# Kernel tuning notes

Measured on AMD Instinct MI355X. Metric: run time of the kernel, lower is better.

Reference implementation:

```python
import jax, jax.numpy as jnp
import numpy as np

B, N, M = 32, 32, 64          # batch, timesteps, local group length (group_token_length+3)
NL, NG = 192, 768             # n_embd_local, n_embd_global
HL, HG = 6, 12                # n_head_local, n_head_global


def setup_inputs() -> dict:
    key = jax.random.key(0)
    ks = jax.random.split(key, 16)
    def w(k, shape, s=0.02):
        return jax.random.normal(k, shape, jnp.float32) * s
    inp = {}
    inp["xl"] = jax.random.normal(ks[0], (B, N, M, NL), jnp.float32)
    inp["xg"] = jax.random.normal(ks[1], (B, 2 * N, NG), jnp.float32)
    i = 2
    for pre, d in (("l", NL), ("g", NG)):
        inp[f"{pre}_ln1_w"] = jnp.ones((d,), jnp.float32)
        inp[f"{pre}_ln1_b"] = jnp.zeros((d,), jnp.float32)
        inp[f"{pre}_ln2_w"] = jnp.ones((d,), jnp.float32)
        inp[f"{pre}_ln2_b"] = jnp.zeros((d,), jnp.float32)
        for nm in ("q", "k", "v", "o"):
            inp[f"{pre}_w{nm}"] = w(ks[i], (d, d)); i += 1
            inp[f"{pre}_b{nm}"] = jnp.zeros((d,), jnp.float32)
        inp[f"{pre}_w1"] = w(ks[i], (d, 4 * d)); i += 1
        inp[f"{pre}_b1"] = jnp.zeros((4 * d,), jnp.float32)
        inp[f"{pre}_w2"] = w(ks[i], (4 * d, d)); i += 1
        inp[f"{pre}_b2"] = jnp.zeros((d,), jnp.float32)
    inp["d_w"] = w(ks[i], (M * NL, NG))
    inp["d_b"] = jnp.zeros((NG,), jnp.float32)
    return inp


def _ln(x, g, b):
    m = x.mean(-1, keepdims=True)
    v = ((x - m) ** 2).mean(-1, keepdims=True)
    return (x - m) / jnp.sqrt(v + 1e-5) * g + b


def _attn(x, wq, bq, wk, bk, wv, bv, wo, bo, nh, allow):
    # x: [B', L, D]; allow: [L, L] bool (True = attend)
    Bx, L, D = x.shape
    hd = D // nh
    q = (x @ wq + bq).reshape(Bx, L, nh, hd)
    k = (x @ wk + bk).reshape(Bx, L, nh, hd)
    v = (x @ wv + bv).reshape(Bx, L, nh, hd)
    s = jnp.einsum('bihd,bjhd->bhij', q, k) / np.float32(np.sqrt(hd))
    s = jnp.where(allow[None, None], s, -jnp.inf)
    p = jax.nn.softmax(s, axis=-1)
    y = jnp.einsum('bhij,bjhd->bihd', p, v).reshape(Bx, L, D)
    return y @ wo + bo


def _tblock(x, p, nh, allow):
    (ln1w, ln1b, ln2w, ln2b, wq, bq, wk, bk, wv, bv, wo, bo, w1, b1, w2, b2) = p
    x = x + _attn(_ln(x, ln1w, ln1b), wq, bq, wk, bk, wv, bv, wo, bo, nh, allow)
    h = _ln(x, ln2w, ln2b)
    return x + (jax.nn.gelu(h @ w1 + b1, approximate=False) @ w2 + b2)


def reference(xl, xg,
              l_ln1_w, l_ln1_b, l_ln2_w, l_ln2_b,
              l_wq, l_bq, l_wk, l_bk, l_wv, l_bv, l_wo, l_bo,
              l_w1, l_b1, l_w2, l_b2,
              g_ln1_w, g_ln1_b, g_ln2_w, g_ln2_b,
              g_wq, g_bq, g_wk, g_bk, g_wv, g_bv, g_wo, g_bo,
              g_w1, g_b1, g_w2, g_b2,
              d_w, d_b):
    Bx, Nx, Mx, nl = xl.shape
    ng = xg.shape[-1]
    lp = (l_ln1_w, l_ln1_b, l_ln2_w, l_ln2_b, l_wq, l_bq, l_wk, l_bk,
          l_wv, l_bv, l_wo, l_bo, l_w1, l_b1, l_w2, l_b2)
    gp = (g_ln1_w, g_ln1_b, g_ln2_w, g_ln2_b, g_wq, g_bq, g_wk, g_bk,
          g_wv, g_bv, g_wo, g_bo, g_w1, g_b1, g_w2, g_b2)

    # local block: causal attention within each group of M tokens
    allow_l = jnp.tril(jnp.ones((Mx, Mx), bool))
    x = _tblock(xl.reshape(Bx * Nx, Mx, nl), lp, HL, allow_l)
    xl_out = x.reshape(Bx, Nx, Mx, nl)

    # summarize each group into one global token, interleave with xg pairs
    zg = (xl_out.reshape(Bx, Nx, Mx * nl) @ d_w + d_b)[:, :, None, :]  # [B,N,1,ng]
    zg = jnp.concatenate([zg, xg.reshape(Bx, Nx, 2, ng)], axis=2)      # [B,N,3,ng]
    zg = zg.reshape(Bx, 3 * Nx, ng)

    # global mask: tril plus within-triplet upper entries; the global block
    # additionally applies its own causal mask, so combined = causal & custom
    L = 3 * Nx
    idx = jnp.arange(L)
    causal = idx[:, None] >= idx[None, :]
    custom = causal | (idx[:, None] // 3 == idx[None, :] // 3)
    allow_g = causal & custom

    zg = _tblock(zg, gp, HG, allow_g)
    xg_out = zg.reshape(Bx, Nx, 3, ng)[:, :, 1:, :].reshape(Bx, 2 * Nx, ng)
    return (xl_out, xg_out)
```

## Files before the change

kernel.cpp:

```cpp
#include <hip/hip_runtime.h>
#include <hip/hip_bf16.h>


typedef unsigned short ushort;
typedef __bf16 bf16x8 __attribute__((ext_vector_type(8)));
typedef float f32x4 __attribute__((ext_vector_type(4)));

__device__ __forceinline__ float us2f(ushort u) {
  union { unsigned i; float f; } w; w.i = ((unsigned)u) << 16; return w.f;
}
__device__ __forceinline__ ushort f2us(float f) {
  __hip_bfloat16 h = __float2bfloat16(f);
  return *reinterpret_cast<ushort*>(&h);
}
__device__ __forceinline__ float gelu_exact(float v) {
  return 0.5f * v * (1.f + erff(v * 0.70710678118654752f));
}
__device__ __forceinline__ void gload16(const ushort* g, ushort* l) {
  __builtin_amdgcn_global_load_lds(
      (const __attribute__((address_space(1))) void*)g,
      (__attribute__((address_space(3))) void*)l, 16, 0, 0);
}

__global__ __launch_bounds__(256)
void transp_kernel(const float* __restrict__ W, ushort* __restrict__ Wt,
                   int K, int N, int dstStride, int rowOff)
{
  __shared__ float t[64][65];
  int n0 = blockIdx.x * 64, k0 = blockIdx.y * 64;
  int c = threadIdx.x & 63, r = threadIdx.x >> 6;
  #pragma unroll
  for (int i = 0; i < 16; ++i) {
    int kr = r + i * 4;
    t[kr][c] = W[(size_t)(k0 + kr) * N + n0 + c];
  }
  __syncthreads();
  #pragma unroll
  for (int i = 0; i < 16; ++i) {
    int nr = r + i * 4;
    Wt[(size_t)(rowOff + n0 + nr) * dstStride + k0 + c] = f2us(t[c][nr]);
  }
}

__global__ __launch_bounds__(256)
void pack3_kernel(float* dst, const float* a, int na, const float* b, int nb,
                  const float* c, int nc)
{
  int i = blockIdx.x * 256 + threadIdx.x;
  if (i >= na + nb + nc) return;
  dst[i] = (i < na) ? a[i] : (i < na + nb ? b[i - na] : c[i - na - nb]);
}

template<int D>
__global__ __launch_bounds__(256)
void ln_kernel(const float* __restrict__ x, const float* __restrict__ g,
               const float* __restrict__ bb, ushort* __restrict__ out, int rows)
{
  int wave = threadIdx.x >> 6, lane = threadIdx.x & 63;
  int row = blockIdx.x * 4 + wave;
  if (row >= rows) return;
  const float* xr = x + (size_t)row * D;
  constexpr int E = D / 64;
  float vals[E];
  float s = 0.f;
  #pragma unroll
  for (int e = 0; e < E; ++e) { vals[e] = xr[e * 64 + lane]; s += vals[e]; }
  #pragma unroll
  for (int off = 32; off >= 1; off >>= 1) s += __shfl_xor(s, off);
  float m = s * (1.f / D);
  float s2 = 0.f;
  #pragma unroll
  for (int e = 0; e < E; ++e) { float d = vals[e] - m; s2 += d * d; }
  #pragma unroll
  for (int off = 32; off >= 1; off >>= 1) s2 += __shfl_xor(s2, off);
  float rstd = rsqrtf(s2 * (1.f / D) + 1e-5f);
  ushort* orow = out + (size_t)row * D;
  #pragma unroll
  for (int e = 0; e < E; ++e) {
    int c = e * 64 + lane;
    orow[c] = f2us((vals[e] - m) * rstd * g[c] + bb[c]);
  }
}

template<int ACT, int RES, int OUTF, int OUTB, int BIAS, int SPLITK>
__global__ __launch_bounds__(256)
void mgemm(const ushort* __restrict__ A, const ushort* __restrict__ Bt,
           const float* __restrict__ bias, const float* __restrict__ resF,
           float* __restrict__ Cf, ushort* __restrict__ Cb,
           int M, int N, int K, int kChunk)
{
  __shared__ __align__(16) ushort Asm[128 * 32];
  __shared__ __align__(16) ushort Bsm[64 * 32];
  const int tid = threadIdx.x;
  const int wave = tid >> 6, lane = tid & 63;
  const int quad = lane >> 4, lm = lane & 15;
  const int rowBase = blockIdx.y * 128, colBase = blockIdx.x * 64;
  const int wrow = (wave & 1) * 64, wcol = (wave >> 1) * 32;
  const int srow = lane >> 2, skcol = (lane & 3) * 8;

  f32x4 acc[4][2] = {};
  const int kbeg = SPLITK ? blockIdx.z * kChunk : 0;
  const int kend = kbeg + (SPLITK ? kChunk : K);

  for (int k0 = kbeg; k0 < kend; k0 += 32) {
    #pragma unroll
    for (int uu = 0; uu < 3; ++uu) {
      int u = wave * 3 + uu;
      if (u < 8) {
        const ushort* gp = A + (size_t)(rowBase + u * 16 + srow) * K + k0 + skcol;
        gload16(gp, &Asm[u * 512]);
      } else {
        int v = u - 8;
        const ushort* gp = Bt + (size_t)(colBase + v * 16 + srow) * K + k0 + skcol;
        gload16(gp, &Bsm[v * 512]);
      }
    }
    __syncthreads();
    bf16x8 af[4], bfr[2];
    #pragma unroll
    for (int r2 = 0; r2 < 4; ++r2)
      af[r2] = *reinterpret_cast<const bf16x8*>(&Asm[(wrow + r2 * 16 + lm) * 32 + quad * 8]);
    #pragma unroll
    for (int c2 = 0; c2 < 2; ++c2)
      bfr[c2] = *reinterpret_cast<const bf16x8*>(&Bsm[(wcol + c2 * 16 + lm) * 32 + quad * 8]);
    #pragma unroll
    for (int r2 = 0; r2 < 4; ++r2)
      #pragma unroll
      for (int c2 = 0; c2 < 2; ++c2)
        acc[r2][c2] = __builtin_amdgcn_mfma_f32_16x16x32_bf16(af[r2], bfr[c2], acc[r2][c2], 0, 0, 0);
    __syncthreads();
  }

  const size_t zoff = SPLITK ? (size_t)blockIdx.z * M * N : 0;
  #pragma unroll
  for (int r2 = 0; r2 < 4; ++r2) {
    #pragma unroll
    for (int c2 = 0; c2 < 2; ++c2) {
      int col = colBase + wcol + c2 * 16 + lm;
      int row0 = rowBase + wrow + r2 * 16 + quad * 4;
      #pragma unroll
      for (int g = 0; g < 4; ++g) {
        float v = acc[r2][c2][g];
        size_t idx = (size_t)(row0 + g) * N + col;
        if (BIAS) v += bias[col];
        if (ACT == 1) v = gelu_exact(v);
        if (RES) v += resF[idx];
        if (OUTF) Cf[zoff + idx] = v;
        if (OUTB) Cb[idx] = f2us(v);
      }
    }
  }
}

__global__ __launch_bounds__(256)
void reduce8_kernel(const float* __restrict__ P, const float* __restrict__ db,
                    float* __restrict__ ZG)
{
  int i = blockIdx.x * 256 + threadIdx.x;
  float s = db[i % 768];
  #pragma unroll
  for (int k = 0; k < 8; ++k) s += P[i + k * 786432];
  ZG[i] = s;
}

template<int L, int HD, int NW>
__global__ __launch_bounds__(NW * 64)
void fattn(const ushort* __restrict__ QKV, ushort* __restrict__ Yp,
           int nh, int DS, int DY, int offQ, int offK, int offV)
{
  constexpr int PQ = HD + 8;
  constexpr int PV = L + 8;
  constexpr int KS = HD / 32;
  constexpr int NCT = L / 16;
  constexpr int KS2 = L / 32;
  constexpr int NYT = HD / 16;
  constexpr int T = NW * 64;
  __shared__ __align__(16) ushort Ql[L * PQ];
  __shared__ __align__(16) ushort Kl[L * PQ];
  __shared__ __align__(16) ushort Vt[HD * PV];
  __shared__ __align__(16) ushort Ps[L * PV];
  const int tid = threadIdx.x;
  const int b = blockIdx.x / nh, h = blockIdx.x % nh;
  const size_t rowb = (size_t)b * L * DS;
  const int hb = h * HD;
  constexpr int CH = L * HD / 8;
  for (int idx = tid; idx < CH; idx += T) {
    int row = idx / (HD / 8), seg = idx % (HD / 8);
    uint4 q4 = *reinterpret_cast<const uint4*>(&QKV[rowb + (size_t)row * DS + offQ + hb + seg * 8]);
    *reinterpret_cast<uint4*>(&Ql[row * PQ + seg * 8]) = q4;
    uint4 k4 = *reinterpret_cast<const uint4*>(&QKV[rowb + (size_t)row * DS + offK + hb + seg * 8]);
    *reinterpret_cast<uint4*>(&Kl[row * PQ + seg * 8]) = k4;
  }
  for (int idx = tid; idx < L * HD; idx += T) {
    int j = idx / HD, d = idx % HD;
    Vt[d * PV + j] = QKV[rowb + (size_t)j * DS + offV + hb + d];
  }
  __syncthreads();
  const int lane = tid & 63;
  const int quad = lane >> 4, lm = lane & 15;
  const int rt = tid >> 6;
  const float scale = rsqrtf((float)HD);
  bf16x8 af[KS];
  #pragma unroll
  for (int s = 0; s < KS; ++s)
    af[s] = *reinterpret_cast<const bf16x8*>(&Ql[(rt * 16 + lm) * PQ + s * 32 + quad * 8]);
  f32x4 sacc[NCT] = {};
  #pragma unroll
  for (int ct = 0; ct < NCT; ++ct)
    #pragma unroll
    for (int s = 0; s < KS; ++s) {
      bf16x8 bf = *reinterpret_cast<const bf16x8*>(&Kl[(ct * 16 + lm) * PQ + s * 32 + quad * 8]);
      sacc[ct] = __builtin_amdgcn_mfma_f32_16x16x32_bf16(af[s], bf, sacc[ct], 0, 0, 0);
    }
  float inv[4];
  #pragma unroll
  for (int g = 0; g < 4; ++g) {
    const int row = rt * 16 + quad * 4 + g;
    float sv[NCT]; float m = -1e30f;
    #pragma unroll
    for (int ct = 0; ct < NCT; ++ct) {
      int col = ct * 16 + lm;
      float x = sacc[ct][g] * scale;
      sv[ct] = (col <= row) ? x : -1e30f;
      m = fmaxf(m, sv[ct]);
    }
    #pragma unroll
    for (int off = 8; off >= 1; off >>= 1) m = fmaxf(m, __shfl_xor(m, off));
    float l = 0.f;
    #pragma unroll
    for (int ct = 0; ct < NCT; ++ct) {
      float p = __expf(sv[ct] - m);
      l += p;
      Ps[row * PV + ct * 16 + lm] = f2us(p);
    }
    #pragma unroll
    for (int off = 8; off >= 1; off >>= 1) l += __shfl_xor(l, off);
    inv[g] = 1.f / l;
  }
  __syncthreads();
  f32x4 yacc[NYT] = {};
  #pragma unroll
  for (int s = 0; s < KS2; ++s) {
    bf16x8 ap = *reinterpret_cast<const bf16x8*>(&Ps[(rt * 16 + lm) * PV + s * 32 + quad * 8]);
    #pragma unroll
    for (int ct = 0; ct < NYT; ++ct) {
      bf16x8 bv = *reinterpret_cast<const bf16x8*>(&Vt[(ct * 16 + lm) * PV + s * 32 + quad * 8]);
      yacc[ct] = __builtin_amdgcn_mfma_f32_16x16x32_bf16(ap, bv, yacc[ct], 0, 0, 0);
    }
  }
  #pragma unroll
  for (int ct = 0; ct < NYT; ++ct)
    #pragma unroll
    for (int g = 0; g < 4; ++g) {
      int row = rt * 16 + quad * 4 + g;
      int d = ct * 16 + lm;
      Yp[((size_t)b * L + row) * DY + hb + d] = f2us(yacc[ct][g] * inv[g]);
    }
}

__global__ __launch_bounds__(256)
void interleave_kernel(const float* __restrict__ zg, const float* __restrict__ xg,
                       float* __restrict__ z)
{
  int idx = blockIdx.x * 256 + threadIdx.x;
  int c = idx % 768;
  int tok = idx / 768;
  int b = tok / 96, r = tok % 96;
  int n = r / 3, t = r % 3;
  z[idx] = (t == 0) ? zg[((size_t)b * 32 + n) * 768 + c]
                    : xg[((size_t)b * 64 + 2 * n + (t - 1)) * 768 + c];
}

__global__ __launch_bounds__(256)
void gather_kernel(const float* __restrict__ zfin, float* __restrict__ dst)
{
  int idx = blockIdx.x * 256 + threadIdx.x;
  int c = idx % 768;
  int t = (idx / 768) % 64;
  int b = idx / (768 * 64);
  int n = t >> 1, s = t & 1;
  dst[idx] = zfin[((size_t)b * 96 + 3 * n + 1 + s) * 768 + c];
}

extern "C" void kernel_launch(void* const* d_in, const int* in_sizes, int n_in,
                              void* d_out, int out_size, void* d_ws, size_t ws_size,
                              hipStream_t stream) {
  const float* xl = (const float*)d_in[0];
  const float* xg = (const float*)d_in[1];
  const float* l_ln1_w = (const float*)d_in[2];  const float* l_ln1_b = (const float*)d_in[3];
  const float* l_ln2_w = (const float*)d_in[4];  const float* l_ln2_b = (const float*)d_in[5];
  const float* l_wq = (const float*)d_in[6];     const float* l_bq = (const float*)d_in[7];
  const float* l_wk = (const float*)d_in[8];     const float* l_bk = (const float*)d_in[9];
  const float* l_wv = (const float*)d_in[10];    const float* l_bv = (const float*)d_in[11];
  const float* l_wo = (const float*)d_in[12];    const float* l_bo = (const float*)d_in[13];
  const float* l_w1 = (const float*)d_in[14];    const float* l_b1 = (const float*)d_in[15];
  const float* l_w2 = (const float*)d_in[16];    const float* l_b2 = (const float*)d_in[17];
  const float* g_ln1_w = (const float*)d_in[18]; const float* g_ln1_b = (const float*)d_in[19];
  const float* g_ln2_w = (const float*)d_in[20]; const float* g_ln2_b = (const float*)d_in[21];
  const float* g_wq = (const float*)d_in[22];    const float* g_bq = (const float*)d_in[23];
  const float* g_wk = (const float*)d_in[24];    const float* g_bk = (const float*)d_in[25];
  const float* g_wv = (const float*)d_in[26];    const float* g_bv = (const float*)d_in[27];
  const float* g_wo = (const float*)d_in[28];    const float* g_bo = (const float*)d_in[29];
  const float* g_w1 = (const float*)d_in[30];    const float* g_b1 = (const float*)d_in[31];
  const float* g_w2 = (const float*)d_in[32];    const float* g_b2 = (const float*)d_in[33];
  const float* dw   = (const float*)d_in[34];    const float* db   = (const float*)d_in[35];

  float* outL = (float*)d_out;
  float* outG = outL + 12582912;

  char* W = (char*)d_ws;
  ushort* A_bf   = (ushort*)(W + 0);
  ushort* QKVl   = (ushort*)(W + 25165824);
  ushort* HIDl   = (ushort*)(W + 25165824);
  ushort* XLb    = (ushort*)(W + 75497472);
  float*  X1     = (float*)(W + 100663296);
  ushort* wqkv_t = (ushort*)(W + 150994944);
  ushort* wo_t   = (ushort*)(W + 151216128);
  ushort* w1_t   = (ushort*)(W + 151289856);
  ushort* w2_t   = (ushort*)(W + 151584768);
  ushort* wd_t   = (ushort*)(W + 151879680);
  ushort* wgqkv_t= (ushort*)(W + 170754048);
  ushort* wgo_t  = (ushort*)(W + 174292992);
  ushort* wg1_t  = (ushort*)(W + 175472640);
  ushort* wg2_t  = (ushort*)(W + 180191232);
  float*  bqkv_l = (float*)(W + 184909824);
  float*  bqkv_g = (float*)(W + 184912128);
  float*  ZGP  = (float*)(W + 0);
  float*  ZG   = (float*)(W + 25165824);
  float*  Z    = (float*)(W + 28311552);
  ushort* LNG  = (ushort*)(W + 37748736);
  ushort* QKVg = (ushort*)(W + 42467328);
  ushort* YG   = (ushort*)(W + 56623104);
  float*  X1G  = (float*)(W + 61341696);
  ushort* HLNG = (ushort*)(W + 70778880);
  ushort* HIDg = (ushort*)(W + 100663296);
  float*  OUTG = (float*)(W + 119537664);

  transp_kernel<<<dim3(3,3),   256, 0, stream>>>(l_wq, wqkv_t, 192, 192, 192, 0);
  transp_kernel<<<dim3(3,3),   256, 0, stream>>>(l_wk, wqkv_t, 192, 192, 192, 192);
  transp_kernel<<<dim3(3,3),   256, 0, stream>>>(l_wv, wqkv_t, 192, 192, 192, 384);
  transp_kernel<<<dim3(3,3),   256, 0, stream>>>(l_wo, wo_t,   192, 192, 192, 0);
  transp_kernel<<<dim3(12,3),  256, 0, stream>>>(l_w1, w1_t,   192, 768, 192, 0);
  transp_kernel<<<dim3(3,12),  256, 0, stream>>>(l_w2, w2_t,   768, 192, 768, 0);
  transp_kernel<<<dim3(12,192),256, 0, stream>>>(dw,   wd_t,   12288, 768, 12288, 0);
  transp_kernel<<<dim3(12,12), 256, 0, stream>>>(g_wq, wgqkv_t, 768, 768, 768, 0);
  transp_kernel<<<dim3(12,12), 256, 0, stream>>>(g_wk, wgqkv_t, 768, 768, 768, 768);
  transp_kernel<<<dim3(12,12), 256, 0, stream>>>(g_wv, wgqkv_t, 768, 768, 768, 1536);
  transp_kernel<<<dim3(12,12), 256, 0, stream>>>(g_wo, wgo_t,  768, 768, 768, 0);
  transp_kernel<<<dim3(48,12), 256, 0, stream>>>(g_w1, wg1_t,  768, 3072, 768, 0);
  transp_kernel<<<dim3(12,48), 256, 0, stream>>>(g_w2, wg2_t,  3072, 768, 3072, 0);
  pack3_kernel<<<3, 256, 0, stream>>>(bqkv_l, l_bq, 192, l_bk, 192, l_bv, 192);
  pack3_kernel<<<9, 256, 0, stream>>>(bqkv_g, g_bq, 768, g_bk, 768, g_bv, 768);

  ln_kernel<192><<<16384, 256, 0, stream>>>(xl, l_ln1_w, l_ln1_b, A_bf, 65536);
  mgemm<0,0,0,1,1,0><<<dim3(9,512), 256, 0, stream>>>(A_bf, wqkv_t, bqkv_l, nullptr, nullptr, QKVl, 65536, 576, 192, 0);
  fattn<64,32,4><<<6144, 256, 0, stream>>>(QKVl, A_bf, 6, 576, 192, 0, 192, 384);
  mgemm<0,1,1,0,1,0><<<dim3(3,512), 256, 0, stream>>>(A_bf, wo_t, l_bo, xl, X1, nullptr, 65536, 192, 192, 0);
  ln_kernel<192><<<16384, 256, 0, stream>>>(X1, l_ln2_w, l_ln2_b, A_bf, 65536);
  for (int h = 0; h < 2; ++h) {
    size_t ro = (size_t)h * 32768 * 192;
    mgemm<1,0,0,1,1,0><<<dim3(12,256), 256, 0, stream>>>(A_bf + ro, w1_t, l_b1, nullptr, nullptr, HIDl, 32768, 768, 192, 0);
    mgemm<0,1,1,1,1,0><<<dim3(3,256), 256, 0, stream>>>(HIDl, w2_t, l_b2, X1 + ro, outL + ro, XLb + ro, 32768, 192, 768, 0);
  }
  mgemm<0,0,1,0,0,1><<<dim3(12,8,8), 256, 0, stream>>>(XLb, wd_t, nullptr, nullptr, ZGP, nullptr, 1024, 768, 12288, 1536);
  reduce8_kernel<<<3072, 256, 0, stream>>>(ZGP, db, ZG);
  interleave_kernel<<<9216, 256, 0, stream>>>(ZG, xg, Z);
  ln_kernel<768><<<768, 256, 0, stream>>>(Z, g_ln1_w, g_ln1_b, LNG, 3072);
  mgemm<0,0,0,1,1,0><<<dim3(36,24), 256, 0, stream>>>(LNG, wgqkv_t, bqkv_g, nullptr, nullptr, QKVg, 3072, 2304, 768, 0);
  fattn<96,64,6><<<384, 384, 0, stream>>>(QKVg, YG, 12, 2304, 768, 0, 768, 1536);
  mgemm<0,1,1,0,1,0><<<dim3(12,24), 256, 0, stream>>>(YG, wgo_t, g_bo, Z, X1G, nullptr, 3072, 768, 768, 0);
  ln_kernel<768><<<768, 256, 0, stream>>>(X1G, g_ln2_w, g_ln2_b, HLNG, 3072);
  mgemm<1,0,0,1,1,0><<<dim3(48,24), 256, 0, stream>>>(HLNG, wg1_t, g_b1, nullptr, nullptr, HIDg, 3072, 3072, 768, 0);
  mgemm<0,1,1,0,1,0><<<dim3(12,24), 256, 0, stream>>>(HIDg, wg2_t, g_b2, X1G, OUTG, nullptr, 3072, 768, 3072, 0);
  gather_kernel<<<6144, 256, 0, stream>>>(OUTG, outG);
}
```

Baseline: 741.8 us.

## Add 128x128 GEMM tile, split-K global FC2, and batch weight transposes

Adds a 128x128-tile GEMM variant and uses it for the local FC1, the downsample GEMM, global QKV and global FC1, which raises operand reuse per block. The global FC2 GEMM now runs as a 4-way split-K with a separate reduction kernel that adds bias and residual. The 13 weight-transpose launches are merged into one kernel driven by a job table, cutting launch overhead. Larger tiles lower occupancy and parallelism on the smaller GEMMs, and the split-K path writes extra partial sums to memory.

```diff
diff --git a/kernel.cpp b/kernel.cpp
--- a/kernel.cpp
+++ b/kernel.cpp
@@ -6,9 +6,6 @@
 typedef __bf16 bf16x8 __attribute__((ext_vector_type(8)));
 typedef float f32x4 __attribute__((ext_vector_type(4)));
 
-__device__ __forceinline__ float us2f(ushort u) {
-  union { unsigned i; float f; } w; w.i = ((unsigned)u) << 16; return w.f;
-}
 __device__ __forceinline__ ushort f2us(float f) {
   __hip_bfloat16 h = __float2bfloat16(f);
   return *reinterpret_cast<ushort*>(&h);
@@ -22,12 +19,25 @@
       (__attribute__((address_space(3))) void*)l, 16, 0, 0);
 }
 
-__global__ __launch_bounds__(256)
-void transp_kernel(const float* __restrict__ W, ushort* __restrict__ Wt,
-                   int K, int N, int dstStride, int rowOff)
-{
+struct TJobs { const float* s[13]; ushort* d[13]; };
+
+__global__ __launch_bounds__(256)
+void transp_all(TJobs J)
+{
+  static constexpr int NN[13]  = {192,192,192,192,768,192,768,768,768,768,768,3072,768};
+  static constexpr int SS[13]  = {192,192,192,192,192,768,12288,768,768,768,768,768,3072};
+  static constexpr int RO[13]  = {0,192,384,0,0,0,0,0,768,1536,0,0,0};
+  static constexpr int CUM[14] = {0,9,18,27,36,72,108,2412,2556,2700,2844,2988,3564,4140};
   __shared__ float t[64][65];
-  int n0 = blockIdx.x * 64, k0 = blockIdx.y * 64;
+  int bid = blockIdx.x;
+  int j = 0;
+  while (bid >= CUM[j + 1]) ++j;
+  int tIdx = bid - CUM[j];
+  const int N = NN[j], stride = SS[j], rowOff = RO[j];
+  const int nx = N >> 6;
+  const int n0 = (tIdx % nx) * 64, k0 = (tIdx / nx) * 64;
+  const float* W = J.s[j];
+  ushort* Wt = J.d[j];
   int c = threadIdx.x & 63, r = threadIdx.x >> 6;
   #pragma unroll
   for (int i = 0; i < 16; ++i) {
@@ -38,7 +48,7 @@
   #pragma unroll
   for (int i = 0; i < 16; ++i) {
     int nr = r + i * 4;
-    Wt[(size_t)(rowOff + n0 + nr) * dstStride + k0 + c] = f2us(t[c][nr]);
+    Wt[(size_t)(rowOff + n0 + nr) * stride + k0 + c] = f2us(t[c][nr]);
   }
 }
 
@@ -82,12 +92,12 @@
   }
 }
 
-template<int ACT, int RES, int OUTF, int OUTB, int BIAS, int SPLITK>
+template<int ACT, int RES, int OUTF, int OUTB, int BIAS>
 __global__ __launch_bounds__(256)
 void mgemm(const ushort* __restrict__ A, const ushort* __restrict__ Bt,
            const float* __restrict__ bias, const float* __restrict__ resF,
            float* __restrict__ Cf, ushort* __restrict__ Cb,
-           int M, int N, int K, int kChunk)
+           int M, int N, int K)
 {
   __shared__ __align__(16) ushort Asm[128 * 32];
   __shared__ __align__(16) ushort Bsm[64 * 32];
@@ -99,10 +109,7 @@
   const int srow = lane >> 2, skcol = (lane & 3) * 8;
 
   f32x4 acc[4][2] = {};
-  const int kbeg = SPLITK ? blockIdx.z * kChunk : 0;
-  const int kend = kbeg + (SPLITK ? kChunk : K);
-
-  for (int k0 = kbeg; k0 < kend; k0 += 32) {
+  for (int k0 = 0; k0 < K; k0 += 32) {
     #pragma unroll
     for (int uu = 0; uu < 3; ++uu) {
       int u = wave * 3 + uu;
@@ -131,11 +138,80 @@
     __syncthreads();
   }
 
+  #pragma unroll
+  for (int r2 = 0; r2 < 4; ++r2) {
+    #pragma unroll
+    for (int c2 = 0; c2 < 2; ++c2) {
+      int col = colBase + wcol + c2 * 16 + lm;
+      int row0 = rowBase + wrow + r2 * 16 + quad * 4;
+      #pragma unroll
+      for (int g = 0; g < 4; ++g) {
+        float v = acc[r2][c2][g];
+        size_t idx = (size_t)(row0 + g) * N + col;
+        if (BIAS) v += bias[col];
+        if (ACT == 1) v = gelu_exact(v);
+        if (RES) v += resF[idx];
+        if (OUTF) Cf[idx] = v;
+        if (OUTB) Cb[idx] = f2us(v);
+      }
+    }
+  }
+}
+
+template<int ACT, int RES, int OUTF, int OUTB, int BIAS, int SPLITK>
+__global__ __launch_bounds__(256)
+void mgemm128(const ushort* __restrict__ A, const ushort* __restrict__ Bt,
+              const float* __restrict__ bias, const float* __restrict__ resF,
+              float* __restrict__ Cf, ushort* __restrict__ Cb,
+              int M, int N, int K, int kChunk)
+{
+  __shared__ __align__(16) ushort Asm[128 * 32];
+  __shared__ __align__(16) ushort Bsm[128 * 32];
+  const int tid = threadIdx.x;
+  const int wave = tid >> 6, lane = tid & 63;
+  const int quad = lane >> 4, lm = lane & 15;
+  const int rowBase = blockIdx.y * 128, colBase = blockIdx.x * 128;
+  const int wrow = (wave & 1) * 64, wcol = (wave >> 1) * 64;
+  const int srow = lane >> 2, skcol = (lane & 3) * 8;
+
+  f32x4 acc[4][4] = {};
+  const int kbeg = SPLITK ? blockIdx.z * kChunk : 0;
+  const int kend = kbeg + (SPLITK ? kChunk : K);
+
+  for (int k0 = kbeg; k0 < kend; k0 += 32) {
+    #pragma unroll
+    for (int uu = 0; uu < 4; ++uu) {
+      int u = wave * 4 + uu;
+      if (u < 8) {
+        const ushort* gp = A + (size_t)(rowBase + u * 16 + srow) * K + k0 + skcol;
+        gload16(gp, &Asm[u * 512]);
+      } else {
+        int v = u - 8;
+        const ushort* gp = Bt + (size_t)(colBase + v * 16 + srow) * K + k0 + skcol;
+        gload16(gp, &Bsm[v * 512]);
+      }
+    }
+    __syncthreads();
+    bf16x8 af[4], bfr[4];
+    #pragma unroll
+    for (int r2 = 0; r2 < 4; ++r2)
+      af[r2] = *reinterpret_cast<const bf16x8*>(&Asm[(wrow + r2 * 16 + lm) * 32 + quad * 8]);
+    #pragma unroll
+    for (int c2 = 0; c2 < 4; ++c2)
+      bfr[c2] = *reinterpret_cast<const bf16x8*>(&Bsm[(wcol + c2 * 16 + lm) * 32 + quad * 8]);
+    #pragma unroll
+    for (int r2 = 0; r2 < 4; ++r2)
+      #pragma unroll
+      for (int c2 = 0; c2 < 4; ++c2)
+        acc[r2][c2] = __builtin_amdgcn_mfma_f32_16x16x32_bf16(af[r2], bfr[c2], acc[r2][c2], 0, 0, 0);
+    __syncthreads();
+  }
+
   const size_t zoff = SPLITK ? (size_t)blockIdx.z * M * N : 0;
   #pragma unroll
   for (int r2 = 0; r2 < 4; ++r2) {
     #pragma unroll
-    for (int c2 = 0; c2 < 2; ++c2) {
+    for (int c2 = 0; c2 < 4; ++c2) {
       int col = colBase + wcol + c2 * 16 + lm;
       int row0 = rowBase + wrow + r2 * 16 + quad * 4;
       #pragma unroll
@@ -161,6 +237,17 @@
   #pragma unroll
   for (int k = 0; k < 8; ++k) s += P[i + k * 786432];
   ZG[i] = s;
+}
+
+__global__ __launch_bounds__(256)
+void reduce4res_kernel(const float* __restrict__ P, const float* __restrict__ db,
+                       const float* __restrict__ res, float* __restrict__ out)
+{
+  int i = blockIdx.x * 256 + threadIdx.x;
+  float s = db[i % 768] + res[i];
+  #pragma unroll
+  for (int k = 0; k < 4; ++k) s += P[i + k * 2359296];
+  out[i] = s;
 }
 
 template<int L, int HD, int NW>
@@ -326,6 +413,7 @@
   float*  bqkv_l = (float*)(W + 184909824);
   float*  bqkv_g = (float*)(W + 184912128);
   float*  ZGP  = (float*)(W + 0);
+  float*  FC2P = (float*)(W + 0);
   float*  ZG   = (float*)(W + 25165824);
   float*  Z    = (float*)(W + 28311552);
   ushort* LNG  = (ushort*)(W + 37748736);
@@ -336,41 +424,39 @@
   ushort* HIDg = (ushort*)(W + 100663296);
   float*  OUTG = (float*)(W + 119537664);
 
-  transp_kernel<<<dim3(3,3),   256, 0, stream>>>(l_wq, wqkv_t, 192, 192, 192, 0);
-  transp_kernel<<<dim3(3,3),   256, 0, stream>>>(l_wk, wqkv_t, 192, 192, 192, 192);
-  transp_kernel<<<dim3(3,3),   256, 0, stream>>>(l_wv, wqkv_t, 192, 192, 192, 384);
-  transp_kernel<<<dim3(3,3),   256, 0, stream>>>(l_wo, wo_t,   192, 192, 192, 0);
-  transp_kernel<<<dim3(12,3),  256, 0, stream>>>(l_w1, w1_t,   192, 768, 192, 0);
-  transp_kernel<<<dim3(3,12),  256, 0, stream>>>(l_w2, w2_t,   768, 192, 768, 0);
-  transp_kernel<<<dim3(12,192),256, 0, stream>>>(dw,   wd_t,   12288, 768, 12288, 0);
-  transp_kernel<<<dim3(12,12), 256, 0, stream>>>(g_wq, wgqkv_t, 768, 768, 768, 0);
-  transp_kernel<<<dim3(12,12), 256, 0, stream>>>(g_wk, wgqkv_t, 768, 768, 768, 768);
-  transp_kernel<<<dim3(12,12), 256, 0, stream>>>(g_wv, wgqkv_t, 768, 768, 768, 1536);
-  transp_kernel<<<dim3(12,12), 256, 0, stream>>>(g_wo, wgo_t,  768, 768, 768, 0);
-  transp_kernel<<<dim3(48,12), 256, 0, stream>>>(g_w1, wg1_t,  768, 3072, 768, 0);
-  transp_kernel<<<dim3(12,48), 256, 0, stream>>>(g_w2, wg2_t,  3072, 768, 3072, 0);
+  TJobs tj;
+  tj.s[0] = l_wq; tj.s[1] = l_wk; tj.s[2] = l_wv; tj.s[3] = l_wo;
+  tj.s[4] = l_w1; tj.s[5] = l_w2; tj.s[6] = dw;
+  tj.s[7] = g_wq; tj.s[8] = g_wk; tj.s[9] = g_wv; tj.s[10] = g_wo;
+  tj.s[11] = g_w1; tj.s[12] = g_w2;
+  tj.d[0] = wqkv_t; tj.d[1] = wqkv_t; tj.d[2] = wqkv_t; tj.d[3] = wo_t;
+  tj.d[4] = w1_t; tj.d[5] = w2_t; tj.d[6] = wd_t;
+  tj.d[7] = wgqkv_t; tj.d[8] = wgqkv_t; tj.d[9] = wgqkv_t; tj.d[10] = wgo_t;
+  tj.d[11] = wg1_t; tj.d[12] = wg2_t;
+  transp_all<<<4140, 256, 0, stream>>>(tj);
   pack3_kernel<<<3, 256, 0, stream>>>(bqkv_l, l_bq, 192, l_bk, 192, l_bv, 192);
   pack3_kernel<<<9, 256, 0, stream>>>(bqkv_g, g_bq, 768, g_bk, 768, g_bv, 768);
 
   ln_kernel<192><<<16384, 256, 0, stream>>>(xl, l_ln1_w, l_ln1_b, A_bf, 65536);
-  mgemm<0,0,0,1,1,0><<<dim3(9,512), 256, 0, stream>>>(A_bf, wqkv_t, bqkv_l, nullptr, nullptr, QKVl, 65536, 576, 192, 0);
+  mgemm<0,0,0,1,1><<<dim3(9,512), 256, 0, stream>>>(A_bf, wqkv_t, bqkv_l, nullptr, nullptr, QKVl, 65536, 576, 192);
   fattn<64,32,4><<<6144, 256, 0, stream>>>(QKVl, A_bf, 6, 576, 192, 0, 192, 384);
-  mgemm<0,1,1,0,1,0><<<dim3(3,512), 256, 0, stream>>>(A_bf, wo_t, l_bo, xl, X1, nullptr, 65536, 192, 192, 0);
+  mgemm<0,1,1,0,1><<<dim3(3,512), 256, 0, stream>>>(A_bf, wo_t, l_bo, xl, X1, nullptr, 65536, 192, 192);
   ln_kernel<192><<<16384, 256, 0, stream>>>(X1, l_ln2_w, l_ln2_b, A_bf, 65536);
   for (int h = 0; h < 2; ++h) {
     size_t ro = (size_t)h * 32768 * 192;
-    mgemm<1,0,0,1,1,0><<<dim3(12,256), 256, 0, stream>>>(A_bf + ro, w1_t, l_b1, nullptr, nullptr, HIDl, 32768, 768, 192, 0);
-    mgemm<0,1,1,1,1,0><<<dim3(3,256), 256, 0, stream>>>(HIDl, w2_t, l_b2, X1 + ro, outL + ro, XLb + ro, 32768, 192, 768, 0);
-  }
-  mgemm<0,0,1,0,0,1><<<dim3(12,8,8), 256, 0, stream>>>(XLb, wd_t, nullptr, nullptr, ZGP, nullptr, 1024, 768, 12288, 1536);
+    mgemm128<1,0,0,1,1,0><<<dim3(6,256), 256, 0, stream>>>(A_bf + ro, w1_t, l_b1, nullptr, nullptr, HIDl, 32768, 768, 192, 0);
+    mgemm<0,1,1,1,1><<<dim3(3,256), 256, 0, stream>>>(HIDl, w2_t, l_b2, X1 + ro, outL + ro, XLb + ro, 32768, 192, 768);
+  }
+  mgemm128<0,0,1,0,0,1><<<dim3(6,8,8), 256, 0, stream>>>(XLb, wd_t, nullptr, nullptr, ZGP, nullptr, 1024, 768, 12288, 1536);
   reduce8_kernel<<<3072, 256, 0, stream>>>(ZGP, db, ZG);
   interleave_kernel<<<9216, 256, 0, stream>>>(ZG, xg, Z);
   ln_kernel<768><<<768, 256, 0, stream>>>(Z, g_ln1_w, g_ln1_b, LNG, 3072);
-  mgemm<0,0,0,1,1,0><<<dim3(36,24), 256, 0, stream>>>(LNG, wgqkv_t, bqkv_g, nullptr, nullptr, QKVg, 3072, 2304, 768, 0);
+  mgemm128<0,0,0,1,1,0><<<dim3(18,24), 256, 0, stream>>>(LNG, wgqkv_t, bqkv_g, nullptr, nullptr, QKVg, 3072, 2304, 768, 0);
   fattn<96,64,6><<<384, 384, 0, stream>>>(QKVg, YG, 12, 2304, 768, 0, 768, 1536);
-  mgemm<0,1,1,0,1,0><<<dim3(12,24), 256, 0, stream>>>(YG, wgo_t, g_bo, Z, X1G, nullptr, 3072, 768, 768, 0);
+  mgemm<0,1,1,0,1><<<dim3(12,24), 256, 0, stream>>>(YG, wgo_t, g_bo, Z, X1G, nullptr, 3072, 768, 768);
   ln_kernel<768><<<768, 256, 0, stream>>>(X1G, g_ln2_w, g_ln2_b, HLNG, 3072);
-  mgemm<1,0,0,1,1,0><<<dim3(48,24), 256, 0, stream>>>(HLNG, wg1_t, g_b1, nullptr, nullptr, HIDg, 3072, 3072, 768, 0);
-  mgemm<0,1,1,0,1,0><<<dim3(12,24), 256, 0, stream>>>(HIDg, wg2_t, g_b2, X1G, OUTG, nullptr, 3072, 768, 3072, 0);
+  mgemm128<1,0,0,1,1,0><<<dim3(24,24), 256, 0, stream>>>(HLNG, wg1_t, g_b1, nullptr, nullptr, HIDg, 3072, 3072, 768, 0);
+  mgemm128<0,0,1,0,0,1><<<dim3(6,24,4), 256, 0, stream>>>(HIDg, wg2_t, nullptr, nullptr, FC2P, nullptr, 3072, 768, 3072, 768);
+  reduce4res_kernel<<<9216, 256, 0, stream>>>(FC2P, g_b2, X1G, OUTG);
   gather_kernel<<<6144, 256, 0, stream>>>(OUTG, outG);
 }
```

Result: faster. 700.4 us (-5.6%).
